# Optimization experiments

Hardware: AMD Instinct MI355X
Metric: run time of the kernel (lower is better)

## Reference

```python
import jax, jax.numpy as jnp
import numpy as np

N = 8192       # patients (nodes)
E = 262144     # edges per graph (avg degree 32)
DF = 128       # dim_final
SLOPE = 0.25   # leaky_relu negative slope


def _spmm(rows, cols, vals, dense):
    # out[i] = sum_{e: rows[e]==i} vals[e] * dense[cols[e]]  == sparse_adj @ dense
    return jax.ops.segment_sum(vals[:, None] * dense[cols], rows, num_segments=N)


def _branch(x, rows, cols, vals, w1, b1, w2, b2):
    # GraphGCN: gc1 -> leaky_relu -> (dropout: identity in eval) -> gc2 -> leaky_relu
    h = _spmm(rows, cols, vals, x @ w1) + b1
    h = jax.nn.leaky_relu(h, negative_slope=SLOPE)
    h = _spmm(rows, cols, vals, h @ w2) + b2
    return jax.nn.leaky_relu(h, negative_slope=SLOPE)


def setup_inputs() -> dict:
    key = jax.random.key(0)
    ks = jax.random.split(key, 40)
    i = 0

    def xav(k, shape):
        std = (2.0 / (shape[0] + shape[1])) ** 0.5
        return std * jax.random.normal(k, shape, dtype=jnp.float32)

    inp = {}
    feat_dims = {"RNAseq": 4096, "dnam": 4096, "cn": 4096, "mic": 1024}
    for name, d in feat_dims.items():
        inp[name] = jax.random.normal(ks[i], (N, d), dtype=jnp.float32); i += 1
    for g in range(1, 5):
        inp[f"rows{g}"] = jax.random.randint(ks[i], (E,), 0, N, dtype=jnp.int32); i += 1
        inp[f"cols{g}"] = jax.random.randint(ks[i], (E,), 0, N, dtype=jnp.int32); i += 1
        inp[f"vals{g}"] = jax.random.uniform(ks[i], (E,), dtype=jnp.float32); i += 1
    # per-branch params: (in_dim, hid_dim); suffixes r=RNAseq, d=meth, c=CN, m=miRNA
    specs = {"r": (4096, 512), "d": (4096, 512), "c": (4096, 512), "m": (1024, 256)}
    for s, (din, dh) in specs.items():
        inp[f"w1_{s}"] = xav(ks[i], (din, dh)); i += 1
        inp[f"b1_{s}"] = jnp.zeros((dh,), jnp.float32)
        inp[f"w2_{s}"] = xav(ks[i], (dh, DF)); i += 1
        inp[f"b2_{s}"] = jnp.zeros((DF,), jnp.float32)
    return inp


def reference(RNAseq, dnam, cn, mic,
              rows1, cols1, vals1, rows2, cols2, vals2,
              rows3, cols3, vals3, rows4, cols4, vals4,
              w1_r, b1_r, w2_r, b2_r,
              w1_d, b1_d, w2_d, b2_d,
              w1_c, b1_c, w2_c, b2_c,
              w1_m, b1_m, w2_m, b2_m):
    x_r = _branch(RNAseq, rows1, cols1, vals1, w1_r, b1_r, w2_r, b2_r)
    x_d = _branch(dnam,   rows2, cols2, vals2, w1_d, b1_d, w2_d, b2_d)
    x_c = _branch(cn,     rows3, cols3, vals3, w1_c, b1_c, w2_c, b2_c)
    x_m = _branch(mic,    rows4, cols4, vals4, w1_m, b1_m, w2_m, b2_m)
    return (x_r + x_d + x_c + x_m) / 4.0
```

## Files before the change

kernel.cpp:

```cpp
#include <hip/hip_runtime.h>

#define N_NODES 8192
#define N_EDGES 262144
#define SLOPE 0.25f

typedef __attribute__((ext_vector_type(8))) short bf16x8;
typedef __attribute__((ext_vector_type(4))) float f32x4;

__device__ __forceinline__ float lrelu(float x) { return x >= 0.f ? x : SLOPE * x; }

__device__ __forceinline__ unsigned short bf16_rne(float x) {
    unsigned u = __float_as_uint(x);
    return (unsigned short)((u + 0x7FFFu + ((u >> 16) & 1u)) >> 16);
}
__device__ __forceinline__ float bf2f(unsigned short h) {
    return __uint_as_float(((unsigned)h) << 16);
}
__device__ __forceinline__ bf16x8 pack8(const float4& a, const float4& b) {
    bf16x8 r;
    r[0] = (short)bf16_rne(a.x); r[1] = (short)bf16_rne(a.y);
    r[2] = (short)bf16_rne(a.z); r[3] = (short)bf16_rne(a.w);
    r[4] = (short)bf16_rne(b.x); r[5] = (short)bf16_rne(b.y);
    r[6] = (short)bf16_rne(b.z); r[7] = (short)bf16_rne(b.w);
    return r;
}

#define GLDS16(g, l)                                                              \
    __builtin_amdgcn_global_load_lds((const __attribute__((address_space(1))) void*)(g), \
                                     (__attribute__((address_space(3))) void*)(l), 16, 0, 0)

struct TransB { const float* W[4]; unsigned short* Th[4]; int K[4]; int N[4]; };

__global__ __launch_bounds__(256) void tsplit(TransB tb) {
    const int z = blockIdx.z;
    const int K = tb.K[z], N = tb.N[z];
    const int k0 = blockIdx.x * 32, n0 = blockIdx.y * 32;
    if (k0 >= K || n0 >= N) return;
    __shared__ float t[32][33];
    const int tx = threadIdx.x & 31, ty = threadIdx.x >> 5;
    const float* W = tb.W[z];
#pragma unroll
    for (int i = 0; i < 32; i += 8)
        t[ty + i][tx] = W[(size_t)(k0 + ty + i) * N + n0 + tx];
    __syncthreads();
#pragma unroll
    for (int i = 0; i < 32; i += 8) {
        const int n = ty + i;
        tb.Th[z][(size_t)(n0 + n) * K + k0 + tx] = bf16_rne(t[tx][n]);
    }
}

struct GemmB {
    const void* A[4];
    const unsigned short* Bh[4];
    unsigned short* C[4];
    int K[4];
    int NT[4];
};

template <int NF, int AF32>
__global__ __launch_bounds__(256, 2) void gemm_bf16s(GemmB gb) {
    constexpr int BGR = NF / 2;
    const int nwg = gridDim.x * gridDim.y * gridDim.z;
    int id = (blockIdx.z * gridDim.y + blockIdx.y) * gridDim.x + blockIdx.x;
    const int cpx = nwg >> 3;
    id = (id & 7) * cpx + (id >> 3);
    const int by = id % gridDim.y;
    const int rest = id / gridDim.y;
    const int bx = rest % gridDim.x;
    const int z = rest / gridDim.x;

    const int nt = gb.NT[z];
    if (by >= nt) return;
    const int K = gb.K[z];
    const int N = nt * (NF * 32);
    const float* __restrict__ Af = (const float*)gb.A[z];
    const unsigned short* __restrict__ Ab = (const unsigned short*)gb.A[z];
    const unsigned short* __restrict__ Bh = gb.Bh[z];
    unsigned short* __restrict__ C = gb.C[z];

    __shared__ unsigned short As[3 * 4096];
    __shared__ unsigned short Bs[3 * NF * 1024];
    const int tid = threadIdx.x;
    const int w = tid >> 6, lane = tid & 63;
    const int wm = w >> 1, wn = w & 1;
    const int bm0 = bx * 128, bn0 = by * (NF * 32);

    auto stageB = [&](int buf, int kt) {
        const int k0 = kt << 5;
#pragma unroll
        for (int i = 0; i < BGR; ++i) {
            const int f = (w * BGR + i) * 64 + lane;
            const int row = f >> 2, s = f & 3;
            const int kg = s ^ ((row >> 1) & 3);
            GLDS16(Bh + (size_t)(bn0 + row) * K + k0 + kg * 8,
                   &Bs[buf * (NF * 1024) + (w * BGR + i) * 512]);
        }
    };
    auto stageAglds = [&](int buf, int kt) {
        const int k0 = kt << 5;
#pragma unroll
        for (int i = 0; i < 2; ++i) {
            const int f = (w * 2 + i) * 64 + lane;
            const int row = f >> 2, s = f & 3;
            const int kg = s ^ ((row >> 1) & 3);
            GLDS16(Ab + (size_t)(bm0 + row) * K + k0 + kg * 8,
                   &As[buf * 4096 + (w * 2 + i) * 512]);
        }
    };
    auto issueA = [&](float4 (&ar)[2][2], int kt) {
        const int k0 = kt << 5;
#pragma unroll
        for (int i = 0; i < 2; ++i) {
            const int f = i * 256 + tid;
            const int row = f >> 2, s = f & 3;
            const int kg = s ^ ((row >> 1) & 3);
            const float* src = Af + (size_t)(bm0 + row) * K + k0 + kg * 8;
            ar[i][0] = *reinterpret_cast<const float4*>(src);
            ar[i][1] = *reinterpret_cast<const float4*>(src + 4);
        }
    };
    auto writeA = [&](float4 (&ar)[2][2], int buf) {
#pragma unroll
        for (int i = 0; i < 2; ++i)
            *reinterpret_cast<bf16x8*>(&As[buf * 4096 + (i * 256 + tid) * 8]) =
                pack8(ar[i][0], ar[i][1]);
    };

    f32x4 acc[4][NF];
#pragma unroll
    for (int mf = 0; mf < 4; ++mf)
#pragma unroll
        for (int nf = 0; nf < NF; ++nf) acc[mf][nf] = (f32x4){0.f, 0.f, 0.f, 0.f};

    const int nk = K >> 5;
    float4 aE[2][2], aO[2][2];

    if constexpr (AF32) {
        issueA(aE, 0); stageB(0, 0);
        issueA(aO, 1); stageB(1, 1);
        asm volatile("s_waitcnt vmcnt(12)" ::: "memory");
        writeA(aE, 0);
        asm volatile("s_waitcnt lgkmcnt(0)" ::: "memory");
    } else {
        stageAglds(0, 0); stageB(0, 0);
        stageAglds(1, 1); stageB(1, 1);
    }

    auto body = [&](int t, float4 (&iset)[2][2], float4 (&wset)[2][2]) {
        const int cb = t % 3;
        if (t + 2 < nk) {
            if constexpr (AF32) issueA(iset, t + 2);
            else stageAglds((t + 2) % 3, t + 2);
            stageB((t + 2) % 3, t + 2);
            if constexpr (AF32) asm volatile("s_waitcnt vmcnt(16)" ::: "memory");
            else asm volatile("s_waitcnt vmcnt(8)" ::: "memory");
        } else if (t + 1 < nk) {
            if constexpr (AF32) asm volatile("s_waitcnt vmcnt(8)" ::: "memory");
            else asm volatile("s_waitcnt vmcnt(4)" ::: "memory");
        } else {
            asm volatile("s_waitcnt vmcnt(0)" ::: "memory");
        }
        __builtin_amdgcn_s_barrier();
        __builtin_amdgcn_sched_barrier(0);

        if constexpr (AF32) {
            if (t + 1 < nk) {
                if (t + 2 < nk) asm volatile("s_waitcnt vmcnt(12)" ::: "memory");
                else asm volatile("s_waitcnt vmcnt(4)" ::: "memory");
                writeA(wset, (t + 1) % 3);
            }
        }

        const int kq = lane >> 4;
        bf16x8 a[4], b[NF];
#pragma unroll
        for (int mf = 0; mf < 4; ++mf) {
            const int r = wm * 64 + mf * 16 + (lane & 15);
            a[mf] = *reinterpret_cast<const bf16x8*>(
                &As[cb * 4096 + r * 32 + ((kq ^ ((r >> 1) & 3)) << 3)]);
        }
#pragma unroll
        for (int nf = 0; nf < NF; ++nf) {
            const int r = wn * (NF * 16) + nf * 16 + (lane & 15);
            b[nf] = *reinterpret_cast<const bf16x8*>(
                &Bs[cb * (NF * 1024) + r * 32 + ((kq ^ ((r >> 1) & 3)) << 3)]);
        }
        __builtin_amdgcn_s_setprio(1);
#pragma unroll
        for (int mf = 0; mf < 4; ++mf)
#pragma unroll
            for (int nf = 0; nf < NF; ++nf)
                acc[mf][nf] = __builtin_amdgcn_mfma_f32_16x16x32_bf16(a[mf], b[nf], acc[mf][nf], 0, 0, 0);
        __builtin_amdgcn_s_setprio(0);

        asm volatile("s_waitcnt lgkmcnt(0)" ::: "memory");
        __builtin_amdgcn_s_barrier();
    };

    for (int t = 0; t < nk; t += 2) {
        body(t, aE, aO);
        body(t + 1, aO, aE);
    }

    const int cr = (lane >> 4) * 4, cc = lane & 15;
#pragma unroll
    for (int mf = 0; mf < 4; ++mf)
#pragma unroll
        for (int nf = 0; nf < NF; ++nf)
#pragma unroll
            for (int j = 0; j < 4; ++j)
                C[(size_t)(bm0 + wm * 64 + mf * 16 + cr + j) * N + bn0 + wn * (NF * 16) + nf * 16 + cc] =
                    bf16_rne(acc[mf][nf][j]);
}

struct GraphPtrs {
    const int* r[4];
    const int* c[4];
    const float* v[4];
};

__global__ __launch_bounds__(256) void hist4(GraphPtrs p, int* __restrict__ cnt4) {
    const int g = blockIdx.y;
    const int e = blockIdx.x * 256 + threadIdx.x;
    atomicAdd(&cnt4[g * N_NODES + p.r[g][e]], 1);
}

__global__ __launch_bounds__(256) void scan4(const int* __restrict__ cnt4,
                                             int* __restrict__ rs4,
                                             int* __restrict__ cur4) {
    const int g = blockIdx.x;
    const int* cnt = cnt4 + g * N_NODES;
    int* row_start = rs4 + (size_t)g * (N_NODES + 1);
    int* cursor = cur4 + g * N_NODES;
    __shared__ int ssum[256];
    const int t = threadIdx.x;
    int local[32];
    int s = 0;
#pragma unroll
    for (int j = 0; j < 32; ++j) { local[j] = cnt[t * 32 + j]; s += local[j]; }
    ssum[t] = s;
    __syncthreads();
    for (int off = 1; off < 256; off <<= 1) {
        const int v = ssum[t];
        const int add = (t >= off) ? ssum[t - off] : 0;
        __syncthreads();
        ssum[t] = v + add;
        __syncthreads();
    }
    int run = (t == 0) ? 0 : ssum[t - 1];
#pragma unroll
    for (int j = 0; j < 32; ++j) {
        row_start[t * 32 + j] = run;
        cursor[t * 32 + j] = run;
        run += local[j];
    }
    if (t == 255) row_start[N_NODES] = run;
}

__global__ __launch_bounds__(256) void scatter4(GraphPtrs p, int* __restrict__ cur4,
                                                unsigned long long* __restrict__ pe4) {
    const int g = blockIdx.y;
    const int e = blockIdx.x * 256 + threadIdx.x;
    const int r = p.r[g][e];
    const int pos = atomicAdd(&cur4[g * N_NODES + r], 1);
    pe4[(size_t)g * N_EDGES + pos] =
        (unsigned long long)(unsigned)p.c[g][e] |
        ((unsigned long long)__float_as_uint(p.v[g][e]) << 32);
}

struct SpmmB {
    const int* rs[4];
    const unsigned long long* pe[4];
    const unsigned short* Y[4];
    const float* bi[4];
    unsigned short* H[4];
};

template <int NC>
__global__ __launch_bounds__(256) void spmm_h1(SpmmB sb) {
    constexpr int PL = NC / 64;
    const int z = blockIdx.y;
    const int row = (blockIdx.x * 256 + threadIdx.x) >> 6;
    const int lane = threadIdx.x & 63;
    const int* rs = sb.rs[z];
    const int s = rs[row], e1 = rs[row + 1];
    const unsigned long long* pe = sb.pe[z];
    const unsigned short* Y = sb.Y[z];
    const int base = lane * PL;

    float acc[PL];
#pragma unroll
    for (int j = 0; j < PL; ++j) acc[j] = 0.f;
    for (int e = s; e < e1; ++e) {
        const unsigned long long ev = pe[e];
        const int c = (int)(unsigned)ev;
        const float v = __uint_as_float((unsigned)(ev >> 32));
        const unsigned short* y = Y + (size_t)c * NC + base;
        if constexpr (PL == 8) {
            const bf16x8 raw = *reinterpret_cast<const bf16x8*>(y);
#pragma unroll
            for (int j = 0; j < 8; ++j)
                acc[j] = fmaf(v, bf2f((unsigned short)raw[j]), acc[j]);
        } else {
            const ushort4 raw = *reinterpret_cast<const ushort4*>(y);
            acc[0] = fmaf(v, bf2f(raw.x), acc[0]);
            acc[1] = fmaf(v, bf2f(raw.y), acc[1]);
            acc[2] = fmaf(v, bf2f(raw.z), acc[2]);
            acc[3] = fmaf(v, bf2f(raw.w), acc[3]);
        }
    }
    const float* bi = sb.bi[z];
    unsigned short* H = sb.H[z] + (size_t)row * NC + base;
    if constexpr (PL == 8) {
        bf16x8 vh;
#pragma unroll
        for (int j = 0; j < 8; ++j) vh[j] = (short)bf16_rne(lrelu(acc[j] + bi[base + j]));
        *reinterpret_cast<bf16x8*>(H) = vh;
    } else {
        ushort4 vh;
        vh.x = bf16_rne(lrelu(acc[0] + bi[base + 0]));
        vh.y = bf16_rne(lrelu(acc[1] + bi[base + 1]));
        vh.z = bf16_rne(lrelu(acc[2] + bi[base + 2]));
        vh.w = bf16_rne(lrelu(acc[3] + bi[base + 3]));
        *reinterpret_cast<ushort4*>(H) = vh;
    }
}

struct Out4 { const float* b2[4]; };

__global__ __launch_bounds__(256) void spmm_out4(const int* __restrict__ rs4,
                                                 const unsigned long long* __restrict__ pe4,
                                                 const unsigned short* __restrict__ Y2all,
                                                 Out4 ob, float* __restrict__ out) {
    const int row = (blockIdx.x * 256 + threadIdx.x) >> 6;
    const int lane = threadIdx.x & 63;
    const int base = lane * 2;
    float r0 = 0.f, r1 = 0.f;
#pragma unroll
    for (int b = 0; b < 4; ++b) {
        const int* rs = rs4 + (size_t)b * (N_NODES + 1);
        const int s = rs[row], e1 = rs[row + 1];
        const unsigned long long* pe = pe4 + (size_t)b * N_EDGES;
        const unsigned short* Y = Y2all + (size_t)b * N_NODES * 128;
        float a0 = 0.f, a1 = 0.f;
        for (int e = s; e < e1; ++e) {
            const unsigned long long ev = pe[e];
            const float v = __uint_as_float((unsigned)(ev >> 32));
            const unsigned u = *reinterpret_cast<const unsigned*>(
                Y + (size_t)(unsigned)ev * 128 + base);
            a0 = fmaf(v, __uint_as_float(u << 16), a0);
            a1 = fmaf(v, __uint_as_float(u & 0xFFFF0000u), a1);
        }
        const float* bi = ob.b2[b];
        r0 += lrelu(a0 + bi[base]);
        r1 += lrelu(a1 + bi[base + 1]);
    }
    *reinterpret_cast<float2*>(out + (size_t)row * 128 + base) =
        make_float2(0.25f * r0, 0.25f * r1);
}

__global__ __launch_bounds__(256) void spmm_out1(const int* __restrict__ rs,
                                                 const unsigned long long* __restrict__ pe,
                                                 const unsigned short* __restrict__ Y,
                                                 const float* __restrict__ bias,
                                                 float* __restrict__ out, int first) {
    const int row = (blockIdx.x * 256 + threadIdx.x) >> 6;
    const int lane = threadIdx.x & 63;
    const int base = lane * 2;
    const int s = rs[row], e1 = rs[row + 1];
    float a0 = 0.f, a1 = 0.f;
    for (int e = s; e < e1; ++e) {
        const unsigned long long ev = pe[e];
        const float v = __uint_as_float((unsigned)(ev >> 32));
        const unsigned u = *reinterpret_cast<const unsigned*>(
            Y + (size_t)(unsigned)ev * 128 + base);
        a0 = fmaf(v, __uint_as_float(u << 16), a0);
        a1 = fmaf(v, __uint_as_float(u & 0xFFFF0000u), a1);
    }
    float r0 = 0.25f * lrelu(a0 + bias[base]);
    float r1 = 0.25f * lrelu(a1 + bias[base + 1]);
    float* o = out + (size_t)row * 128 + base;
    if (!first) {
        const float2 p = *reinterpret_cast<const float2*>(o);
        r0 += p.x;
        r1 += p.y;
    }
    *reinterpret_cast<float2*>(o) = make_float2(r0, r1);
}

extern "C" void kernel_launch(void* const* d_in, const int* in_sizes, int n_in,
                              void* d_out, int out_size, void* d_ws, size_t ws_size,
                              hipStream_t stream) {
    const float* X[4] = {(const float*)d_in[0], (const float*)d_in[1],
                         (const float*)d_in[2], (const float*)d_in[3]};
    GraphPtrs gp;
    for (int b = 0; b < 4; ++b) {
        gp.r[b] = (const int*)d_in[4 + 3 * b];
        gp.c[b] = (const int*)d_in[5 + 3 * b];
        gp.v[b] = (const float*)d_in[6 + 3 * b];
    }
    const float *w1[4], *b1[4], *w2[4], *b2[4];
    for (int b = 0; b < 4; ++b) {
        w1[b] = (const float*)d_in[16 + 4 * b + 0];
        b1[b] = (const float*)d_in[16 + 4 * b + 1];
        w2[b] = (const float*)d_in[16 + 4 * b + 2];
        b2[b] = (const float*)d_in[16 + 4 * b + 3];
    }
    const int din[4] = {4096, 4096, 4096, 1024};
    const int dh[4] = {512, 512, 512, 256};
    float* out = (float*)d_out;

    char* wsc = (char*)d_ws;
    size_t off = 0;
    auto carve = [&](size_t bytes) {
        void* p = wsc + off;
        off += (bytes + 255) & ~(size_t)255;
        return p;
    };
    int* cnt4 = (int*)carve((size_t)4 * N_NODES * 4);
    int* rs4 = (int*)carve((size_t)4 * (N_NODES + 1) * 4);
    int* cur4 = (int*)carve((size_t)4 * N_NODES * 4);
    unsigned long long* pe4 = (unsigned long long*)carve((size_t)4 * N_EDGES * 8);

    size_t tier1_base = off;
    unsigned short *W1h[4], *W2h[4], *Y1[4], *H1[4];
    for (int b = 0; b < 4; ++b) W1h[b] = (unsigned short*)carve((size_t)dh[b] * din[b] * 2);
    for (int b = 0; b < 4; ++b) W2h[b] = (unsigned short*)carve((size_t)128 * dh[b] * 2);
    for (int b = 0; b < 4; ++b) Y1[b] = (unsigned short*)carve((size_t)N_NODES * dh[b] * 2);
    for (int b = 0; b < 4; ++b) H1[b] = (unsigned short*)carve((size_t)N_NODES * dh[b] * 2);
    unsigned short* Y2all = (unsigned short*)carve((size_t)4 * N_NODES * 128 * 2);
    const bool tier1 = (off <= ws_size);
    unsigned short* Y2s[4];
    if (tier1) {
        for (int b = 0; b < 4; ++b) Y2s[b] = Y2all + (size_t)b * N_NODES * 128;
    } else {
        off = tier1_base;
        unsigned short* w1h = (unsigned short*)carve((size_t)512 * 4096 * 2);
        unsigned short* w2h = (unsigned short*)carve((size_t)128 * 512 * 2);
        unsigned short* y1 = (unsigned short*)carve((size_t)N_NODES * 512 * 2);
        unsigned short* h1 = (unsigned short*)carve((size_t)N_NODES * 512 * 2);
        unsigned short* y2 = (unsigned short*)carve((size_t)N_NODES * 128 * 2);
        for (int b = 0; b < 4; ++b) {
            W1h[b] = w1h; W2h[b] = w2h;
            Y1[b] = y1; H1[b] = h1; Y2s[b] = y2;
        }
    }

    hipMemsetAsync(cnt4, 0, (size_t)4 * N_NODES * sizeof(int), stream);
    {
        dim3 g(N_EDGES / 256, 4);
        hist4<<<g, 256, 0, stream>>>(gp, cnt4);
        scan4<<<4, 256, 0, stream>>>(cnt4, rs4, cur4);
        scatter4<<<g, 256, 0, stream>>>(gp, cur4, pe4);
    }

    if (tier1) {
        TransB t1;
        for (int b = 0; b < 4; ++b) {
            t1.W[b] = w1[b]; t1.Th[b] = W1h[b];
            t1.K[b] = din[b]; t1.N[b] = dh[b];
        }
        tsplit<<<dim3(128, 16, 4), 256, 0, stream>>>(t1);

        GemmB g1;
        for (int b = 0; b < 4; ++b) {
            g1.A[b] = X[b]; g1.Bh[b] = W1h[b];
            g1.C[b] = Y1[b]; g1.K[b] = din[b]; g1.NT[b] = dh[b] / 256;
        }
        gemm_bf16s<8, 1><<<dim3(64, 2, 4), 256, 0, stream>>>(g1);

        SpmmB s1;
        for (int b = 0; b < 4; ++b) {
            s1.rs[b] = rs4 + (size_t)b * (N_NODES + 1);
            s1.pe[b] = pe4 + (size_t)b * N_EDGES;
            s1.Y[b] = Y1[b]; s1.bi[b] = b1[b]; s1.H[b] = H1[b];
        }
        spmm_h1<512><<<dim3(N_NODES / 4, 3), 256, 0, stream>>>(s1);
        SpmmB s1m = s1;
        s1m.rs[0] = s1.rs[3]; s1m.pe[0] = s1.pe[3];
        s1m.Y[0] = s1.Y[3]; s1m.bi[0] = s1.bi[3]; s1m.H[0] = s1.H[3];
        spmm_h1<256><<<dim3(N_NODES / 4, 1), 256, 0, stream>>>(s1m);

        TransB t2;
        for (int b = 0; b < 4; ++b) {
            t2.W[b] = w2[b]; t2.Th[b] = W2h[b];
            t2.K[b] = dh[b]; t2.N[b] = 128;
        }
        tsplit<<<dim3(16, 4, 4), 256, 0, stream>>>(t2);

        GemmB g2;
        for (int b = 0; b < 4; ++b) {
            g2.A[b] = H1[b]; g2.Bh[b] = W2h[b];
            g2.C[b] = Y2s[b]; g2.K[b] = dh[b]; g2.NT[b] = 1;
        }
        gemm_bf16s<4, 0><<<dim3(64, 1, 4), 256, 0, stream>>>(g2);

        Out4 ob;
        for (int b = 0; b < 4; ++b) ob.b2[b] = b2[b];
        spmm_out4<<<N_NODES / 4, 256, 0, stream>>>(rs4, pe4, Y2all, ob, out);
    } else {
        for (int b = 0; b < 4; ++b) {
            TransB t1;
            t1.W[0] = w1[b]; t1.Th[0] = W1h[b];
            t1.K[0] = din[b]; t1.N[0] = dh[b];
            tsplit<<<dim3(din[b] / 32, dh[b] / 32, 1), 256, 0, stream>>>(t1);
            GemmB g1;
            g1.A[0] = X[b]; g1.Bh[0] = W1h[b];
            g1.C[0] = Y1[b]; g1.K[0] = din[b]; g1.NT[0] = dh[b] / 256;
            gemm_bf16s<8, 1><<<dim3(64, dh[b] / 256, 1), 256, 0, stream>>>(g1);
            SpmmB s1;
            s1.rs[0] = rs4 + (size_t)b * (N_NODES + 1);
            s1.pe[0] = pe4 + (size_t)b * N_EDGES;
            s1.Y[0] = Y1[b]; s1.bi[0] = b1[b]; s1.H[0] = H1[b];
            if (dh[b] == 512)
                spmm_h1<512><<<dim3(N_NODES / 4, 1), 256, 0, stream>>>(s1);
            else
                spmm_h1<256><<<dim3(N_NODES / 4, 1), 256, 0, stream>>>(s1);
            TransB t2;
            t2.W[0] = w2[b]; t2.Th[0] = W2h[b];
            t2.K[0] = dh[b]; t2.N[0] = 128;
            tsplit<<<dim3(dh[b] / 32, 4, 1), 256, 0, stream>>>(t2);
            GemmB g2;
            g2.A[0] = H1[b]; g2.Bh[0] = W2h[b];
            g2.C[0] = Y2s[b]; g2.K[0] = dh[b]; g2.NT[0] = 1;
            gemm_bf16s<4, 0><<<dim3(64, 1, 1), 256, 0, stream>>>(g2);
            spmm_out1<<<N_NODES / 4, 256, 0, stream>>>(
                rs4 + (size_t)b * (N_NODES + 1), pe4 + (size_t)b * N_EDGES,
                Y2s[b], b2[b], out, b == 0);
        }
    }
}
```

Before: 533.1 us.

## Merge layer-1 SpMM launches into one XCD-aware kernel pinning branches to L2

Replaces the two separate layer-1 SpMM launches (three 512-wide branches plus one 256-wide) with a single kernel of 8192 blocks. Block IDs are decoded so that each pair of XCDs (blocks are assigned round-robin across the 8 XCDs) serves only one graph branch. Each branch's gathered Y1 rows therefore stay in fewer L2 caches, and the extra launch and the tail between launches go away. The cost is a runtime branch on the column width and a dependence on the hardware's block-to-XCD mapping. The fallback kernel also now takes plain pointer arguments instead of the struct.

Result: no change. 526.7 us (-1.2%).

```diff
diff --git a/kernel.cpp b/kernel.cpp
--- a/kernel.cpp
+++ b/kernel.cpp
@@ -275,28 +275,83 @@
     const unsigned short* Y[4];
     const float* bi[4];
     unsigned short* H[4];
+    int nc[4];
 };
 
-template <int NC>
-__global__ __launch_bounds__(256) void spmm_h1(SpmmB sb) {
-    constexpr int PL = NC / 64;
-    const int z = blockIdx.y;
-    const int row = (blockIdx.x * 256 + threadIdx.x) >> 6;
+__global__ __launch_bounds__(256) void spmm_h1x(SpmmB sb) {
+    const int id = blockIdx.x;
+    const int xcd = id & 7;
+    const int z = xcd >> 1;
+    const int rb = ((id >> 3) << 1) + (id & 1);
+    const int row = rb * 4 + (threadIdx.x >> 6);
     const int lane = threadIdx.x & 63;
+    const int nc = sb.nc[z];
     const int* rs = sb.rs[z];
     const int s = rs[row], e1 = rs[row + 1];
     const unsigned long long* pe = sb.pe[z];
     const unsigned short* Y = sb.Y[z];
+    const float* bi = sb.bi[z];
+
+    if (nc == 512) {
+        const int base = lane * 8;
+        float acc[8];
+#pragma unroll
+        for (int j = 0; j < 8; ++j) acc[j] = 0.f;
+        for (int e = s; e < e1; ++e) {
+            const unsigned long long ev = pe[e];
+            const float v = __uint_as_float((unsigned)(ev >> 32));
+            const bf16x8 raw = *reinterpret_cast<const bf16x8*>(
+                Y + (size_t)(unsigned)ev * 512 + base);
+#pragma unroll
+            for (int j = 0; j < 8; ++j)
+                acc[j] = fmaf(v, bf2f((unsigned short)raw[j]), acc[j]);
+        }
+        bf16x8 vh;
+#pragma unroll
+        for (int j = 0; j < 8; ++j) vh[j] = (short)bf16_rne(lrelu(acc[j] + bi[base + j]));
+        *reinterpret_cast<bf16x8*>(sb.H[z] + (size_t)row * 512 + base) = vh;
+    } else {
+        const int base = lane * 4;
+        float acc[4];
+#pragma unroll
+        for (int j = 0; j < 4; ++j) acc[j] = 0.f;
+        for (int e = s; e < e1; ++e) {
+            const unsigned long long ev = pe[e];
+            const float v = __uint_as_float((unsigned)(ev >> 32));
+            const ushort4 raw = *reinterpret_cast<const ushort4*>(
+                Y + (size_t)(unsigned)ev * 256 + base);
+            acc[0] = fmaf(v, bf2f(raw.x), acc[0]);
+            acc[1] = fmaf(v, bf2f(raw.y), acc[1]);
+            acc[2] = fmaf(v, bf2f(raw.z), acc[2]);
+            acc[3] = fmaf(v, bf2f(raw.w), acc[3]);
+        }
+        ushort4 vh;
+        vh.x = bf16_rne(lrelu(acc[0] + bi[base + 0]));
+        vh.y = bf16_rne(lrelu(acc[1] + bi[base + 1]));
+        vh.z = bf16_rne(lrelu(acc[2] + bi[base + 2]));
+        vh.w = bf16_rne(lrelu(acc[3] + bi[base + 3]));
+        *reinterpret_cast<ushort4*>(sb.H[z] + (size_t)row * 256 + base) = vh;
+    }
+}
+
+template <int NC>
+__global__ __launch_bounds__(256) void spmm_h1(const int* __restrict__ rs,
+                                               const unsigned long long* __restrict__ pe,
+                                               const unsigned short* __restrict__ Y,
+                                               const float* __restrict__ bi,
+                                               unsigned short* __restrict__ Hd) {
+    constexpr int PL = NC / 64;
+    const int row = (blockIdx.x * 256 + threadIdx.x) >> 6;
+    const int lane = threadIdx.x & 63;
+    const int s = rs[row], e1 = rs[row + 1];
     const int base = lane * PL;
-
     float acc[PL];
 #pragma unroll
     for (int j = 0; j < PL; ++j) acc[j] = 0.f;
     for (int e = s; e < e1; ++e) {
         const unsigned long long ev = pe[e];
-        const int c = (int)(unsigned)ev;
         const float v = __uint_as_float((unsigned)(ev >> 32));
-        const unsigned short* y = Y + (size_t)c * NC + base;
+        const unsigned short* y = Y + (size_t)(unsigned)ev * NC + base;
         if constexpr (PL == 8) {
             const bf16x8 raw = *reinterpret_cast<const bf16x8*>(y);
 #pragma unroll
@@ -310,8 +365,7 @@
             acc[3] = fmaf(v, bf2f(raw.w), acc[3]);
         }
     }
-    const float* bi = sb.bi[z];
-    unsigned short* H = sb.H[z] + (size_t)row * NC + base;
+    unsigned short* H = Hd + (size_t)row * NC + base;
     if constexpr (PL == 8) {
         bf16x8 vh;
 #pragma unroll
@@ -475,12 +529,9 @@
             s1.rs[b] = rs4 + (size_t)b * (N_NODES + 1);
             s1.pe[b] = pe4 + (size_t)b * N_EDGES;
             s1.Y[b] = Y1[b]; s1.bi[b] = b1[b]; s1.H[b] = H1[b];
-        }
-        spmm_h1<512><<<dim3(N_NODES / 4, 3), 256, 0, stream>>>(s1);
-        SpmmB s1m = s1;
-        s1m.rs[0] = s1.rs[3]; s1m.pe[0] = s1.pe[3];
-        s1m.Y[0] = s1.Y[3]; s1m.bi[0] = s1.bi[3]; s1m.H[0] = s1.H[3];
-        spmm_h1<256><<<dim3(N_NODES / 4, 1), 256, 0, stream>>>(s1m);
+            s1.nc[b] = dh[b];
+        }
+        spmm_h1x<<<8192, 256, 0, stream>>>(s1);
 
         TransB t2;
         for (int b = 0; b < 4; ++b) {
@@ -509,14 +560,14 @@
             g1.A[0] = X[b]; g1.Bh[0] = W1h[b];
             g1.C[0] = Y1[b]; g1.K[0] = din[b]; g1.NT[0] = dh[b] / 256;
             gemm_bf16s<8, 1><<<dim3(64, dh[b] / 256, 1), 256, 0, stream>>>(g1);
-            SpmmB s1;
-            s1.rs[0] = rs4 + (size_t)b * (N_NODES + 1);
-            s1.pe[0] = pe4 + (size_t)b * N_EDGES;
-            s1.Y[0] = Y1[b]; s1.bi[0] = b1[b]; s1.H[0] = H1[b];
             if (dh[b] == 512)
-                spmm_h1<512><<<dim3(N_NODES / 4, 1), 256, 0, stream>>>(s1);
+                spmm_h1<512><<<N_NODES / 4, 256, 0, stream>>>(
+                    rs4 + (size_t)b * (N_NODES + 1), pe4 + (size_t)b * N_EDGES,
+                    Y1[b], b1[b], H1[b]);
             else
-                spmm_h1<256><<<dim3(N_NODES / 4, 1), 256, 0, stream>>>(s1);
+                spmm_h1<256><<<N_NODES / 4, 256, 0, stream>>>(
+                    rs4 + (size_t)b * (N_NODES + 1), pe4 + (size_t)b * N_EDGES,
+                    Y1[b], b1[b], H1[b]);
             TransB t2;
             t2.W[0] = w2[b]; t2.Th[0] = W2h[b];
             t2.K[0] = dh[b]; t2.N[0] = 128;
```
